# Optimization experiments

Hardware: AMD Instinct MI355X
Metric: run time of the kernel (lower is better)

## Reference

```python
import jax, jax.numpy as jnp
import numpy as np

D_MODEL = 1024
N_HEADS = 16
HEAD_DIM = D_MODEL // N_HEADS


def setup_inputs() -> dict:
    key = jax.random.key(0)
    k0, k1, k2, k3, k4, k5 = jax.random.split(key, 6)
    s = 1.0 / np.sqrt(D_MODEL)
    return {
        "q": jax.random.normal(k0, (2, 2048, D_MODEL), dtype=jnp.float32),
        "Wq": jax.random.normal(k1, (D_MODEL, D_MODEL), dtype=jnp.float32) * s,
        "Wk": jax.random.normal(k2, (D_MODEL, D_MODEL), dtype=jnp.float32) * s,
        "Wv": jax.random.normal(k3, (D_MODEL, D_MODEL), dtype=jnp.float32) * s,
        "Wo": jax.random.normal(k4, (D_MODEL, D_MODEL), dtype=jnp.float32) * s,
        "bo": jax.random.normal(k5, (D_MODEL,), dtype=jnp.float32) * 0.01,
    }


def _split_heads(x):
    b, s, _ = x.shape
    return x.reshape(b, s, N_HEADS, HEAD_DIM).transpose(0, 2, 1, 3)  # [b,h,s,d]


def reference(q, Wq, Wk, Wv, Wo, bo):
    # self-attention: k = v = q
    qh = _split_heads(q @ Wq)  # [b,h,s,d]
    kh = _split_heads(q @ Wk)
    vh = _split_heads(q @ Wv)
    scale = 1.0 / np.sqrt(HEAD_DIM).astype(np.float32)
    scores = jnp.einsum("bhqd,bhkd->bhqk", qh, kh) * scale
    attn = jax.nn.softmax(scores, axis=-1)
    ctx = jnp.einsum("bhqk,bhkd->bhqd", attn, vh)
    b, h, s, d = ctx.shape
    ctx = ctx.transpose(0, 2, 1, 3).reshape(b, s, h * d)
    return ctx @ Wo + bo
```

## Files before the change

kernel.cpp:

```cpp
#include <hip/hip_runtime.h>
#include <cstdint>

typedef unsigned short u16;
typedef __bf16 bf16x8 __attribute__((ext_vector_type(8)));
typedef __bf16 bf16x2 __attribute__((ext_vector_type(2)));
typedef float floatx4 __attribute__((ext_vector_type(4)));
typedef unsigned short u16x4 __attribute__((ext_vector_type(4)));
typedef unsigned short u16x8 __attribute__((ext_vector_type(8)));

#define MFMA16(a, b, c) __builtin_amdgcn_mfma_f32_16x16x32_bf16((a), (b), (c), 0, 0, 0)
#define QSCALE_LOG2E 0.18033688011112042f


typedef __attribute__((address_space(3))) void as3_void;
typedef __attribute__((address_space(1))) void as1_void;

static __device__ __forceinline__ void async_load16(const void* g, void* l) {
  __builtin_amdgcn_global_load_lds((as1_void*)(uintptr_t)g, (as3_void*)(uintptr_t)l,
                                   16, 0, 0);
}

static __device__ __forceinline__ u16 f2bf(float f) {
  union { float f; unsigned int u; } v; v.f = f;
  unsigned int u = v.u;
  u += 0x7fffu + ((u >> 16) & 1u);
  return (u16)(u >> 16);
}

static __device__ __forceinline__ u16x4 pack_bf4(float a, float b, float c, float d) {
#if __has_builtin(__builtin_amdgcn_cvt_pk_bf16_f32)
  union { u16x4 v4; bf16x2 v2[2]; } u;
  u.v2[0] = __builtin_amdgcn_cvt_pk_bf16_f32(a, b);
  u.v2[1] = __builtin_amdgcn_cvt_pk_bf16_f32(c, d);
  return u.v4;
#else
  u16x4 r; r[0] = f2bf(a); r[1] = f2bf(b); r[2] = f2bf(c); r[3] = f2bf(d);
  return r;
#endif
}

static __device__ __forceinline__ float fast_exp2(float x) {
#if __has_builtin(__builtin_amdgcn_exp2f)
  return __builtin_amdgcn_exp2f(x);
#else
  return exp2f(x);
#endif
}


__global__ __launch_bounds__(256) void prep_kernel(
    const float* __restrict__ w0, const float* __restrict__ w1,
    const float* __restrict__ w2, const float* __restrict__ w3,
    u16* __restrict__ wout,
    const float* __restrict__ xin, u16* __restrict__ xout) {
  if (blockIdx.z == 4) {
    int blk = blockIdx.y * 16 + blockIdx.x;
    size_t base = (size_t)blk * 16384 + (size_t)threadIdx.x * 8;
#pragma unroll
    for (int r = 0; r < 8; r++) {
      size_t i = base + (size_t)r * 2048;
      float4 a = *(const float4*)(xin + i);
      float4 b = *(const float4*)(xin + i + 4);
      u16x8 o;
      o[0] = f2bf(a.x); o[1] = f2bf(a.y); o[2] = f2bf(a.z); o[3] = f2bf(a.w);
      o[4] = f2bf(b.x); o[5] = f2bf(b.y); o[6] = f2bf(b.z); o[7] = f2bf(b.w);
      *(u16x8*)(xout + i) = o;
    }
    return;
  }
  __shared__ u16 t[64][65];
  const float* in = (blockIdx.z == 0) ? w0 : (blockIdx.z == 1) ? w1
                    : (blockIdx.z == 2) ? w2 : w3;
  u16* oz = wout + (size_t)blockIdx.z * (1024 * 1024);
  const int tid = threadIdx.x;
  const int x = tid & 63, y0 = tid >> 6;
  const int bx = blockIdx.x * 64, by = blockIdx.y * 64;
#pragma unroll
  for (int p = 0; p < 16; p++) {
    int y = y0 + p * 4;
    t[y][x] = f2bf(in[(size_t)(by + y) * 1024 + bx + x]);
  }
  __syncthreads();
#pragma unroll
  for (int p = 0; p < 16; p++) {
    int r = y0 + p * 4;
    oz[(size_t)(bx + r) * 1024 + by + x] = t[x][r];
  }
}


__global__ __launch_bounds__(256) void transpose_bf16_kernel(
    const u16* __restrict__ in, u16* __restrict__ out, int R, int C) {
  __shared__ u16 t[64][65];
  const int tid = threadIdx.x;
  const int x = tid & 63, y0 = tid >> 6;
  const size_t zo = (size_t)blockIdx.z * (size_t)R * (size_t)C;
  const u16* iz = in + zo;
  u16* oz = out + zo;
  const int bx = blockIdx.x * 64, by = blockIdx.y * 64;
#pragma unroll
  for (int p = 0; p < 16; p++) {
    int y = y0 + p * 4;
    t[y][x] = iz[(size_t)(by + y) * C + bx + x];
  }
  __syncthreads();
#pragma unroll
  for (int p = 0; p < 16; p++) {
    int r = y0 + p * 4;
    oz[(size_t)(bx + r) * R + by + x] = t[x][r];
  }
}


__global__ __launch_bounds__(256, 2) void gemm_bt_kernel(
    const u16* __restrict__ A, const u16* __restrict__ BT,
    const float* __restrict__ bias, void* __restrict__ out,
    int M, int N, int K, int mode) {
  __shared__ u16 As[128 * 32];
  __shared__ u16 Bs[128 * 32];
  const int tid = threadIdx.x;
  const int w = tid >> 6, lane = tid & 63;
  const int bm = blockIdx.y * 128, bn = blockIdx.x * 128;
  const int z = blockIdx.z;
  const u16* Bz = BT + (size_t)z * N * K;

  const int c0 = w * 2, c1 = c0 + 1;
  const int mA0 = c0 * 16 + (lane >> 2), mA1 = c1 * 16 + (lane >> 2);
  const int kg0 = (lane & 3) ^ ((mA0 >> 1) & 3);
  const int kg1 = (lane & 3) ^ ((mA1 >> 1) & 3);
  const u16* agp0 = A + (size_t)(bm + mA0) * K + kg0 * 8;
  const u16* agp1 = A + (size_t)(bm + mA1) * K + kg1 * 8;
  const u16* bgp0 = Bz + (size_t)(bn + mA0) * K + kg0 * 8;
  const u16* bgp1 = Bz + (size_t)(bn + mA1) * K + kg1 * 8;
  u16* ald0 = As + c0 * 512; u16* ald1 = As + c1 * 512;
  u16* bld0 = Bs + c0 * 512; u16* bld1 = Bs + c1 * 512;

  const int wm = (w >> 1) * 64, wn = (w & 1) * 64;
  floatx4 acc[4][4] = {};

  int a_off[4], b_off[4];
#pragma unroll
  for (int i = 0; i < 4; i++) {
    int m = wm + i * 16 + (lane & 15);
    a_off[i] = m * 32 + (((lane >> 4) ^ ((m >> 1) & 3)) * 8);
    int n = wn + i * 16 + (lane & 15);
    b_off[i] = n * 32 + (((lane >> 4) ^ ((n >> 1) & 3)) * 8);
  }

  for (int k0 = 0; k0 < K; k0 += 32) {
    __syncthreads();
    async_load16(agp0 + k0, ald0);
    async_load16(agp1 + k0, ald1);
    async_load16(bgp0 + k0, bld0);
    async_load16(bgp1 + k0, bld1);
    __syncthreads();
    bf16x8 af[4], bf[4];
#pragma unroll
    for (int i = 0; i < 4; i++) af[i] = *(const bf16x8*)(As + a_off[i]);
#pragma unroll
    for (int j = 0; j < 4; j++) bf[j] = *(const bf16x8*)(Bs + b_off[j]);
#pragma unroll
    for (int i = 0; i < 4; i++)
#pragma unroll
      for (int j = 0; j < 4; j++)
        acc[i][j] = MFMA16(af[i], bf[j], acc[i][j]);
  }

  const int roff = (lane >> 4) * 4;
  const int coff = lane & 15;
  if (mode == 0) {
    const float sc = (z == 0) ? QSCALE_LOG2E : 1.0f;
    u16* outz = (u16*)out + (size_t)z * M * N;
#pragma unroll
    for (int i = 0; i < 4; i++) {
      int r0 = bm + wm + i * 16 + roff;
#pragma unroll
      for (int j = 0; j < 4; j++) {
        int c = bn + wn + j * 16 + coff;
        int h = c >> 6, d = c & 63;
#pragma unroll
        for (int r = 0; r < 4; r++) {
          int rr = r0 + r;
          size_t o = ((size_t)((rr >> 11) * 16 + h) * 2048 + (rr & 2047)) * 64 + d;
          outz[o] = f2bf(acc[i][j][r] * sc);
        }
      }
    }
  } else {
    float* outf = (float*)out;
#pragma unroll
    for (int i = 0; i < 4; i++) {
      int r0 = bm + wm + i * 16 + roff;
#pragma unroll
      for (int j = 0; j < 4; j++) {
        int c = bn + wn + j * 16 + coff;
        float bv = bias[c];
#pragma unroll
        for (int r = 0; r < 4; r++)
          outf[(size_t)(r0 + r) * N + c] = acc[i][j][r] + bv;
      }
    }
  }
}


__global__ __launch_bounds__(256, 3) void attn_kernel(
    const u16* __restrict__ Q, const u16* __restrict__ Kx,
    const u16* __restrict__ VT, u16* __restrict__ ctx) {
  __shared__ u16 Ks[128 * 64];
  __shared__ u16 Vs[64 * 128];
  __shared__ u16 Ps[4][16 * 136];
  const int tid = threadIdx.x;
  const int w = tid >> 6, lane = tid & 63;
  const int bh = blockIdx.y;
  const int q0 = blockIdx.x * 64;
  const u16* Qh = Q + (size_t)bh * (2048 * 64);
  const u16* Kh = Kx + (size_t)bh * (2048 * 64);
  const u16* Vh = VT + (size_t)bh * (64 * 2048);

  const int qbase = q0 + w * 16;
  bf16x8 qf[2];
#pragma unroll
  for (int ks = 0; ks < 2; ks++)
    qf[ks] = *(const bf16x8*)(Qh + (size_t)(qbase + (lane & 15)) * 64 +
                              ks * 32 + (lane >> 4) * 8);

  bf16x8 onesf;
#pragma unroll
  for (int i = 0; i < 8; i++) onesf[i] = (__bf16)1.0f;

  const u16* kgp[4]; const u16* vgp[4];
  u16* kld[4]; u16* vld[4];
#pragma unroll
  for (int i = 0; i < 4; i++) {
    int c = w * 4 + i;
    int sl = c * 8 + (lane >> 3);
    int dg = (lane & 7) ^ (lane >> 3);
    kgp[i] = Kh + (size_t)sl * 64 + dg * 8;
    kld[i] = Ks + c * 512;
    int dl = c * 4 + (lane >> 4);
    int sg = (lane & 15) ^ (dl & 15);
    vgp[i] = Vh + (size_t)dl * 2048 + sg * 8;
    vld[i] = Vs + c * 512;
  }

  floatx4 o[4] = {};
  floatx4 lacc = {};
  u16* Pw = Ps[w];

  for (int t = 0; t < 16; t++) {
    const int k0 = t * 128;
    __syncthreads();
#pragma unroll
    for (int i = 0; i < 4; i++) {
      async_load16(kgp[i] + (size_t)k0 * 64, kld[i]);
      async_load16(vgp[i] + k0, vld[i]);
    }
    __syncthreads();

    floatx4 st[8];
#pragma unroll
    for (int si = 0; si < 8; si++) st[si] = floatx4{0.f, 0.f, 0.f, 0.f};
#pragma unroll
    for (int ks = 0; ks < 2; ks++) {
#pragma unroll
      for (int si = 0; si < 8; si++) {
        int s = si * 16 + (lane & 15);
        int slot = ((ks * 4) + (lane >> 4)) ^ (s & 7);
        bf16x8 kf = *(const bf16x8*)(Ks + s * 64 + slot * 8);
        st[si] = MFMA16(kf, qf[ks], st[si]);
      }
    }

    {
      int q = lane & 15;
#pragma unroll
      for (int si = 0; si < 8; si++) {
        float p0 = fast_exp2(st[si][0]);
        float p1 = fast_exp2(st[si][1]);
        float p2 = fast_exp2(st[si][2]);
        float p3 = fast_exp2(st[si][3]);
        u16x4 pk = pack_bf4(p0, p1, p2, p3);
        *(u16x4*)(Pw + q * 136 + si * 16 + (lane >> 4) * 4) = pk;
      }
    }

#pragma unroll
    for (int ks = 0; ks < 4; ks++) {
      bf16x8 vf[4];
#pragma unroll
      for (int jt = 0; jt < 4; jt++) {
        int d = jt * 16 + (lane & 15);
        int slot = ((ks * 4) + (lane >> 4)) ^ (d & 15);
        vf[jt] = *(const bf16x8*)(Vs + d * 128 + slot * 8);
      }
      bf16x8 pf = *(const bf16x8*)(Pw + (lane & 15) * 136 +
                                   ks * 32 + (lane >> 4) * 8);
#pragma unroll
      for (int jt = 0; jt < 4; jt++)
        o[jt] = MFMA16(pf, vf[jt], o[jt]);
      lacc = MFMA16(pf, onesf, lacc);
    }
  }

  const int b = bh >> 4, h = bh & 15;
#pragma unroll
  for (int r = 0; r < 4; r++) {
    float inv = 1.0f / lacc[r];
    int s = qbase + (lane >> 4) * 4 + r;
#pragma unroll
    for (int j = 0; j < 4; j++) {
      int c = h * 64 + j * 16 + (lane & 15);
      ctx[(size_t)(b * 2048 + s) * 1024 + c] = f2bf(o[j][r] * inv);
    }
  }
}


extern "C" void kernel_launch(void* const* d_in, const int* in_sizes, int n_in,
                              void* d_out, int out_size, void* d_ws, size_t ws_size,
                              hipStream_t stream) {
  (void)in_sizes; (void)n_in; (void)out_size; (void)ws_size;
  const float* x  = (const float*)d_in[0];
  const float* Wq = (const float*)d_in[1];
  const float* Wk = (const float*)d_in[2];
  const float* Wv = (const float*)d_in[3];
  const float* Wo = (const float*)d_in[4];
  const float* bo = (const float*)d_in[5];
  u16* ws = (u16*)d_ws;
  const size_t MM = 1024 * 1024;
  u16* WT  = ws;
  u16* WoT = ws + 3 * MM;
  u16* Xb  = ws + 4 * MM;
  u16* QKV = ws + 8 * MM;
  u16* VTp = ws + 20 * MM;
  u16* CTX = ws + 24 * MM;

  dim3 blk(256);
  prep_kernel<<<dim3(16, 16, 5), blk, 0, stream>>>(Wq, Wk, Wv, Wo, WT, x, Xb);
  gemm_bt_kernel<<<dim3(8, 32, 3), blk, 0, stream>>>(Xb, WT, nullptr, QKV,
                                                     4096, 1024, 1024, 0);
  transpose_bf16_kernel<<<dim3(1, 32, 32), blk, 0, stream>>>(QKV + 8 * MM, VTp, 2048, 64);
  attn_kernel<<<dim3(32, 32, 1), blk, 0, stream>>>(QKV, QKV + 4 * MM, VTp, CTX);
  gemm_bt_kernel<<<dim3(8, 32, 1), blk, 0, stream>>>(CTX, WoT, bo, d_out,
                                                     4096, 1024, 1024, 1);
}
```

Measured before the change: 202.1 us.

## Process 32 queries per wave in attention and keep QKV row-major

Each attention wave now handles two 16-query tiles, so every K/V tile staged in LDS serves 128 queries instead of 64. This halves the grid and the K/V global loads and LDS staging per query. The QKV projection epilogue now writes plain row-major [token, d_model] instead of a head-split layout. The attention and V-transpose kernels read with a 1024 stride, which gives simpler, more coalesced GEMM stores. The trade-off is higher register and LDS use, with occupancy hint lowered from 3 to 2 blocks, and fewer blocks to fill the GPU.

```diff
diff --git a/kernel.cpp b/kernel.cpp
--- a/kernel.cpp
+++ b/kernel.cpp
@@ -89,25 +89,25 @@
 }
 
 
-__global__ __launch_bounds__(256) void transpose_bf16_kernel(
-    const u16* __restrict__ in, u16* __restrict__ out, int R, int C) {
+__global__ __launch_bounds__(256) void vt_kernel(
+    const u16* __restrict__ V, u16* __restrict__ VT) {
   __shared__ u16 t[64][65];
+  const int bh = blockIdx.z, b = bh >> 4, h = bh & 15;
+  const u16* iz = V + (size_t)b * 2048 * 1024 + h * 64;
+  u16* oz = VT + (size_t)bh * 64 * 2048;
   const int tid = threadIdx.x;
   const int x = tid & 63, y0 = tid >> 6;
-  const size_t zo = (size_t)blockIdx.z * (size_t)R * (size_t)C;
-  const u16* iz = in + zo;
-  u16* oz = out + zo;
-  const int bx = blockIdx.x * 64, by = blockIdx.y * 64;
+  const int by = blockIdx.y * 64;
 #pragma unroll
   for (int p = 0; p < 16; p++) {
     int y = y0 + p * 4;
-    t[y][x] = iz[(size_t)(by + y) * C + bx + x];
+    t[y][x] = iz[(size_t)(by + y) * 1024 + x];
   }
   __syncthreads();
 #pragma unroll
   for (int p = 0; p < 16; p++) {
     int r = y0 + p * 4;
-    oz[(size_t)(bx + r) * R + by + x] = t[x][r];
+    oz[(size_t)r * 2048 + by + x] = t[x][r];
   }
 }
 
@@ -177,13 +177,9 @@
 #pragma unroll
       for (int j = 0; j < 4; j++) {
         int c = bn + wn + j * 16 + coff;
-        int h = c >> 6, d = c & 63;
-#pragma unroll
-        for (int r = 0; r < 4; r++) {
-          int rr = r0 + r;
-          size_t o = ((size_t)((rr >> 11) * 16 + h) * 2048 + (rr & 2047)) * 64 + d;
-          outz[o] = f2bf(acc[i][j][r] * sc);
-        }
+#pragma unroll
+        for (int r = 0; r < 4; r++)
+          outz[(size_t)(r0 + r) * N + c] = f2bf(acc[i][j][r] * sc);
       }
     }
   } else {
@@ -204,26 +200,28 @@
 }
 
 
-__global__ __launch_bounds__(256, 3) void attn_kernel(
+__global__ __launch_bounds__(256, 2) void attn_kernel(
     const u16* __restrict__ Q, const u16* __restrict__ Kx,
     const u16* __restrict__ VT, u16* __restrict__ ctx) {
   __shared__ u16 Ks[128 * 64];
   __shared__ u16 Vs[64 * 128];
-  __shared__ u16 Ps[4][16 * 136];
+  __shared__ u16 Ps[4][32 * 136];
   const int tid = threadIdx.x;
   const int w = tid >> 6, lane = tid & 63;
-  const int bh = blockIdx.y;
-  const int q0 = blockIdx.x * 64;
-  const u16* Qh = Q + (size_t)bh * (2048 * 64);
-  const u16* Kh = Kx + (size_t)bh * (2048 * 64);
-  const u16* Vh = VT + (size_t)bh * (64 * 2048);
-
-  const int qbase = q0 + w * 16;
-  bf16x8 qf[2];
-#pragma unroll
-  for (int ks = 0; ks < 2; ks++)
-    qf[ks] = *(const bf16x8*)(Qh + (size_t)(qbase + (lane & 15)) * 64 +
-                              ks * 32 + (lane >> 4) * 8);
+  const int bh = blockIdx.y, b = bh >> 4, h = bh & 15;
+  const int q0 = blockIdx.x * 128;
+  const u16* Qh = Q + (size_t)b * 2048 * 1024 + h * 64;
+  const u16* Kh = Kx + (size_t)b * 2048 * 1024 + h * 64;
+  const u16* Vh = VT + (size_t)bh * 64 * 2048;
+
+  const int qbase = q0 + w * 32;
+  bf16x8 qf[2][2];
+#pragma unroll
+  for (int qt = 0; qt < 2; qt++)
+#pragma unroll
+    for (int ks = 0; ks < 2; ks++)
+      qf[qt][ks] = *(const bf16x8*)(Qh + (size_t)(qbase + qt * 16 + (lane & 15)) * 1024 +
+                                    ks * 32 + (lane >> 4) * 8);
 
   bf16x8 onesf;
 #pragma unroll
@@ -236,7 +234,7 @@
     int c = w * 4 + i;
     int sl = c * 8 + (lane >> 3);
     int dg = (lane & 7) ^ (lane >> 3);
-    kgp[i] = Kh + (size_t)sl * 64 + dg * 8;
+    kgp[i] = Kh + (size_t)sl * 1024 + dg * 8;
     kld[i] = Ks + c * 512;
     int dl = c * 4 + (lane >> 4);
     int sg = (lane & 15) ^ (dl & 15);
@@ -244,8 +242,8 @@
     vld[i] = Vs + c * 512;
   }
 
-  floatx4 o[4] = {};
-  floatx4 lacc = {};
+  floatx4 o[2][4] = {};
+  floatx4 lacc[2] = {};
   u16* Pw = Ps[w];
 
   for (int t = 0; t < 16; t++) {
@@ -253,14 +251,17 @@
     __syncthreads();
 #pragma unroll
     for (int i = 0; i < 4; i++) {
-      async_load16(kgp[i] + (size_t)k0 * 64, kld[i]);
+      async_load16(kgp[i] + (size_t)k0 * 1024, kld[i]);
       async_load16(vgp[i] + k0, vld[i]);
     }
     __syncthreads();
 
-    floatx4 st[8];
-#pragma unroll
-    for (int si = 0; si < 8; si++) st[si] = floatx4{0.f, 0.f, 0.f, 0.f};
+    floatx4 st[8][2];
+#pragma unroll
+    for (int si = 0; si < 8; si++) {
+      st[si][0] = floatx4{0.f, 0.f, 0.f, 0.f};
+      st[si][1] = floatx4{0.f, 0.f, 0.f, 0.f};
+    }
 #pragma unroll
     for (int ks = 0; ks < 2; ks++) {
 #pragma unroll
@@ -268,18 +269,20 @@
         int s = si * 16 + (lane & 15);
         int slot = ((ks * 4) + (lane >> 4)) ^ (s & 7);
         bf16x8 kf = *(const bf16x8*)(Ks + s * 64 + slot * 8);
-        st[si] = MFMA16(kf, qf[ks], st[si]);
-      }
-    }
-
-    {
-      int q = lane & 15;
+        st[si][0] = MFMA16(kf, qf[0][ks], st[si][0]);
+        st[si][1] = MFMA16(kf, qf[1][ks], st[si][1]);
+      }
+    }
+
+#pragma unroll
+    for (int qt = 0; qt < 2; qt++) {
+      int q = qt * 16 + (lane & 15);
 #pragma unroll
       for (int si = 0; si < 8; si++) {
-        float p0 = fast_exp2(st[si][0]);
-        float p1 = fast_exp2(st[si][1]);
-        float p2 = fast_exp2(st[si][2]);
-        float p3 = fast_exp2(st[si][3]);
+        float p0 = fast_exp2(st[si][qt][0]);
+        float p1 = fast_exp2(st[si][qt][1]);
+        float p2 = fast_exp2(st[si][qt][2]);
+        float p3 = fast_exp2(st[si][qt][3]);
         u16x4 pk = pack_bf4(p0, p1, p2, p3);
         *(u16x4*)(Pw + q * 136 + si * 16 + (lane >> 4) * 4) = pk;
       }
@@ -294,26 +297,30 @@
         int slot = ((ks * 4) + (lane >> 4)) ^ (d & 15);
         vf[jt] = *(const bf16x8*)(Vs + d * 128 + slot * 8);
       }
-      bf16x8 pf = *(const bf16x8*)(Pw + (lane & 15) * 136 +
-                                   ks * 32 + (lane >> 4) * 8);
-#pragma unroll
-      for (int jt = 0; jt < 4; jt++)
-        o[jt] = MFMA16(pf, vf[jt], o[jt]);
-      lacc = MFMA16(pf, onesf, lacc);
-    }
-  }
-
-  const int b = bh >> 4, h = bh & 15;
-#pragma unroll
-  for (int r = 0; r < 4; r++) {
-    float inv = 1.0f / lacc[r];
-    int s = qbase + (lane >> 4) * 4 + r;
-#pragma unroll
-    for (int j = 0; j < 4; j++) {
-      int c = h * 64 + j * 16 + (lane & 15);
-      ctx[(size_t)(b * 2048 + s) * 1024 + c] = f2bf(o[j][r] * inv);
-    }
-  }
+#pragma unroll
+      for (int qt = 0; qt < 2; qt++) {
+        bf16x8 pf = *(const bf16x8*)(Pw + (qt * 16 + (lane & 15)) * 136 +
+                                     ks * 32 + (lane >> 4) * 8);
+#pragma unroll
+        for (int jt = 0; jt < 4; jt++)
+          o[qt][jt] = MFMA16(pf, vf[jt], o[qt][jt]);
+        lacc[qt] = MFMA16(pf, onesf, lacc[qt]);
+      }
+    }
+  }
+
+#pragma unroll
+  for (int qt = 0; qt < 2; qt++)
+#pragma unroll
+    for (int r = 0; r < 4; r++) {
+      float inv = 1.0f / lacc[qt][r];
+      int s = qbase + qt * 16 + (lane >> 4) * 4 + r;
+#pragma unroll
+      for (int j = 0; j < 4; j++) {
+        int c = h * 64 + j * 16 + (lane & 15);
+        ctx[(size_t)(b * 2048 + s) * 1024 + c] = f2bf(o[qt][j][r] * inv);
+      }
+    }
 }
 
 
@@ -340,8 +347,8 @@
   prep_kernel<<<dim3(16, 16, 5), blk, 0, stream>>>(Wq, Wk, Wv, Wo, WT, x, Xb);
   gemm_bt_kernel<<<dim3(8, 32, 3), blk, 0, stream>>>(Xb, WT, nullptr, QKV,
                                                      4096, 1024, 1024, 0);
-  transpose_bf16_kernel<<<dim3(1, 32, 32), blk, 0, stream>>>(QKV + 8 * MM, VTp, 2048, 64);
-  attn_kernel<<<dim3(32, 32, 1), blk, 0, stream>>>(QKV, QKV + 4 * MM, VTp, CTX);
+  vt_kernel<<<dim3(1, 32, 32), blk, 0, stream>>>(QKV + 8 * MM, VTp);
+  attn_kernel<<<dim3(16, 32, 1), blk, 0, stream>>>(QKV, QKV + 4 * MM, VTp, CTX);
   gemm_bt_kernel<<<dim3(8, 32, 1), blk, 0, stream>>>(CTX, WoT, bo, d_out,
                                                      4096, 1024, 1024, 1);
 }
```

After: 197.7 us. 2.1% less time.
